# Optimization experiments

Hardware: AMD Instinct MI355X
Metric: run time of the kernel (lower is better)

Reference implementation:

```python
import jax, jax.numpy as jnp
from jax import lax
import numpy as np

B, L1, L2 = 64, 1024, 1024


def setup_inputs() -> dict:
    key = jax.random.key(0)
    ks = jax.random.split(key, 6)
    s1 = 1.0 / np.sqrt(L1)
    s2 = 1.0 / np.sqrt(L2)
    return {
        "a": jax.random.normal(ks[0], (B, L1), dtype=jnp.float32),
        "b": jax.random.normal(ks[1], (B, L2), dtype=jnp.float32),
        # nn.Linear(L1, L1) and nn.Linear(L2, L2) params (PyTorch default uniform init range)
        "W1": jax.random.uniform(ks[2], (L1, L1), jnp.float32, -s1, s1),
        "b1": jax.random.uniform(ks[3], (L1,), jnp.float32, -s1, s1),
        "W2": jax.random.uniform(ks[4], (L2, L2), jnp.float32, -s2, s2),
        "b2": jax.random.uniform(ks[5], (L2,), jnp.float32, -s2, s2),
    }


def _dtw_cost(cost):
    """DTW accumulated-cost DP for one [N, M] pairwise-cost matrix.

    R[i,j] = cost[i,j] + min(R[i-1,j-1], R[i-1,j], R[i,j-1]).
    The within-row dependency x[j] = c[j] + min(m[j], x[j-1]) is a min-plus
    prefix: x[j] = S[j] + cummin(m - S_{j-1}) with S = cumsum(c), which lets
    each row be computed in parallel (wavefront-equivalent vectorization).
    Returns the scalar DTW distance R[N-1, M-1].
    """
    dt = cost.dtype
    row0 = jnp.cumsum(cost[0])  # R[0, :]

    def step(prev_row, c_row):
        # m[j] = min(R[i-1, j], R[i-1, j-1]);  j=0 has no (i-1, j-1) neighbor
        shifted = jnp.concatenate([jnp.full((1,), jnp.inf, dt), prev_row[:-1]])
        m = jnp.minimum(prev_row, shifted)
        S = jnp.cumsum(c_row)
        S_prev = jnp.concatenate([jnp.zeros((1,), dt), S[:-1]])
        row = S + lax.associative_scan(jnp.minimum, m - S_prev)
        return row, None

    last_row, _ = lax.scan(step, row0, cost[1:])
    return last_row[-1]


def reference(a, b, W1, b1, W2, b2):
    # seq1 / seq2 linear projections over the time axis
    a_p = a @ W1.T + b1  # [B, L1]
    b_p = b @ W2.T + b2  # [B, L2]
    # squared-euclidean pairwise cost (scipy.sqeuclidean on scalar elements)
    cost = (a_p[:, :, None] - b_p[:, None, :]) ** 2  # [B, L1, L2]
    return jax.vmap(_dtw_cost)(cost)  # [B] DTW distances
```

## Files before the change

### kernel.cpp

```cpp
#include <hip/hip_runtime.h>
#include <math.h>


#define L 1024
#define BATCH 64

__global__ __launch_bounds__(256) void proj_kernel(
    const float* __restrict__ a, const float* __restrict__ b,
    const float* __restrict__ W1, const float* __restrict__ b1,
    const float* __restrict__ W2, const float* __restrict__ b2,
    float* __restrict__ ap, float* __restrict__ bp, int KC) {
  int part = blockIdx.x >> 7;
  int sub = blockIdx.x & 127;
  const float* X;
  const float* W;
  const float* bias;
  float* out;
  int i0;
  if (sub < 64) {
    X = a; W = W1; bias = b1; out = ap + part * BATCH * L; i0 = sub * 16;
  } else {
    X = b; W = W2; bias = b2; out = bp + part * BATCH * L; i0 = (sub - 64) * 16;
  }

  __shared__ float a_s[64][33];
  __shared__ float w_s[16][33];

  int tid = threadIdx.x;
  int lane_b = tid & 63;
  int iq = tid >> 6;

  float acc[4] = {0.f, 0.f, 0.f, 0.f};

  int kbeg = part * KC;
  int kend = kbeg + KC;
  for (int k0 = kbeg; k0 < kend; k0 += 32) {
    {
      int row = tid >> 2;
      int kl = (tid & 3) * 8;
      const float4* src = reinterpret_cast<const float4*>(&X[row * L + k0 + kl]);
      float4 v0 = src[0];
      float4 v1 = src[1];
      a_s[row][kl + 0] = v0.x; a_s[row][kl + 1] = v0.y;
      a_s[row][kl + 2] = v0.z; a_s[row][kl + 3] = v0.w;
      a_s[row][kl + 4] = v1.x; a_s[row][kl + 5] = v1.y;
      a_s[row][kl + 6] = v1.z; a_s[row][kl + 7] = v1.w;
    }
    {
      int row = tid >> 4;
      int kl = (tid & 15) * 2;
      float2 v = *reinterpret_cast<const float2*>(&W[(i0 + row) * L + k0 + kl]);
      w_s[row][kl] = v.x;
      w_s[row][kl + 1] = v.y;
    }
    __syncthreads();
    #pragma unroll 8
    for (int kl = 0; kl < 32; ++kl) {
      float av = a_s[lane_b][kl];
      #pragma unroll
      for (int m = 0; m < 4; ++m) {
        acc[m] += av * w_s[iq * 4 + m][kl];
      }
    }
    __syncthreads();
  }

  #pragma unroll
  for (int m = 0; m < 4; ++m) {
    int i = i0 + iq * 4 + m;
    float bv = (part == 0) ? bias[i] : 0.f;
    out[lane_b * L + i] = acc[m] + bv;
  }
}


#define NW 4
#define CPL 4
#define KBAR 32
#define OFF 95
#define DMAX (OFF * (NW - 1) + 63)
#define NG 43
#define NSTEPS (NG * KBAR)
#define APPAD (DMAX + NSTEPS + 64)

__device__ __forceinline__ float dpp_shr1(float v, float old) {
  int r = __builtin_amdgcn_update_dpp(__float_as_int(old), __float_as_int(v),
                                      0x138, 0xf, 0xf, false);
  return __int_as_float(r);
}

__device__ __forceinline__ float dpp_shl1(float v) {
  int r = __builtin_amdgcn_update_dpp(__float_as_int(v), __float_as_int(v),
                                      0x130, 0xf, 0xf, false);
  return __int_as_float(r);
}

__device__ __forceinline__ float min3f(float x, float y, float z) {
  float r;
  asm("v_min3_f32 %0, %1, %2, %3" : "=v"(r) : "v"(x), "v"(y), "v"(z));
  return r;
}

__global__ __launch_bounds__(256) void dtw_kernel(const float* __restrict__ app,
                                                  const float* __restrict__ bpp,
                                                  float* __restrict__ out,
                                                  int parts) {
  const int b = blockIdx.x;
  const int tid = threadIdx.x;
  const int w = tid >> 6;
  const int t = tid & 63;
  const int woff = w * OFF;
  const int D = woff + t;
  const float INF = INFINITY;

  __shared__ float ap_pad[APPAD];
  __shared__ float ring[NW - 1][64];

  for (int idx = tid; idx < APPAD; idx += 256) {
    int src = idx - DMAX;
    float v = 0.f;
    if ((unsigned)src < (unsigned)L) {
      v = app[b * L + src];
      for (int p = 1; p < parts; ++p) v += app[p * BATCH * L + b * L + src];
    }
    ap_pad[idx] = v;
  }

  float4 bv = *reinterpret_cast<const float4*>(&bpp[b * L + tid * CPL]);
  for (int p = 1; p < parts; ++p) {
    float4 u = *reinterpret_cast<const float4*>(
        &bpp[p * BATCH * L + b * L + tid * CPL]);
    bv.x += u.x; bv.y += u.y; bv.z += u.z; bv.w += u.w;
  }
  const float bpv0 = bv.x, bpv1 = bv.y, bpv2 = bv.z, bpv3 = bv.w;

  float p0 = INF, p1 = INF, p2 = INF, p3 = INF;
  float right = INF, prev_left = INF;
  float vprod = INF;
  float ringchunk = (w == 0 && t == 0) ? 0.f : INF;
  const float* apl = &ap_pad[DMAX - D];

  __syncthreads();

#define DTW_GROUP(s0v, PRED, FIRSTG)                                         \
  {                                                                          \
    const int s0 = (s0v);                                                    \
    float apf[KBAR];                                                         \
    _Pragma("unroll")                                                        \
    for (int k = 0; k < KBAR; ++k) apf[k] = apl[s0 + k];                     \
    if (w > 0 && t < KBAR)                                                   \
      ringchunk = ring[w - 1][(s0 - woff + t) & 63];                         \
    _Pragma("unroll")                                                        \
    for (int k = 0; k < KBAR; ++k) {                                         \
      float left = dpp_shr1(right, ringchunk);                               \
      ringchunk = dpp_shl1(ringchunk);                                       \
      int ii = s0 + k - D;                                                   \
      if (!(PRED) || ((unsigned)ii < (unsigned)L)) {                         \
        float dprev = prev_left;                                             \
        if ((FIRSTG) && k == 1 && w == 0 && t == 0) dprev = INF;             \
        prev_left = left;                                                    \
        float apv = apf[k];                                                  \
        float d0 = apv - bpv0, d1 = apv - bpv1;                              \
        float d2 = apv - bpv2, d3 = apv - bpv3;                              \
        float x = left, bb;                                                  \
        bb = min3f(p0, dprev, x); x = __builtin_fmaf(d0, d0, bb);            \
        dprev = p0; p0 = x;                                                  \
        bb = min3f(p1, dprev, x); x = __builtin_fmaf(d1, d1, bb);            \
        dprev = p1; p1 = x;                                                  \
        bb = min3f(p2, dprev, x); x = __builtin_fmaf(d2, d2, bb);            \
        dprev = p2; p2 = x;                                                  \
        bb = min3f(p3, dprev, x); x = __builtin_fmaf(d3, d3, bb);            \
        p3 = x;                                                              \
        right = x;                                                           \
      }                                                                      \
      vprod = dpp_shl1(vprod);                                               \
      vprod = (t == 63) ? right : vprod;                                     \
    }                                                                        \
    if (w < NW - 1 && t >= 64 - KBAR)                                        \
      ring[w][(s0 + t - woff - (63 + KBAR)) & 63] = vprod;                   \
    __syncthreads();                                                         \
  }

  for (int g = 0; g < 11; ++g) DTW_GROUP(g * KBAR, true, g == 0);
  for (int g = 11; g < 32; ++g) DTW_GROUP(g * KBAR, false, false);
  for (int g = 32; g < NG; ++g) DTW_GROUP(g * KBAR, true, false);
#undef DTW_GROUP

  if (tid == NW * 64 - 1) out[b] = right;
}

extern "C" void kernel_launch(void* const* d_in, const int* in_sizes, int n_in,
                              void* d_out, int out_size, void* d_ws, size_t ws_size,
                              hipStream_t stream) {
  const float* a  = (const float*)d_in[0];
  const float* b  = (const float*)d_in[1];
  const float* W1 = (const float*)d_in[2];
  const float* b1 = (const float*)d_in[3];
  const float* W2 = (const float*)d_in[4];
  const float* b2 = (const float*)d_in[5];
  float* out = (float*)d_out;

  size_t per_part = (size_t)2 * BATCH * L * sizeof(float);
  int parts = 1;
  if (ws_size >= 4 * per_part) parts = 4;
  else if (ws_size >= 2 * per_part) parts = 2;

  float* ap = (float*)d_ws;
  float* bp = ap + (size_t)parts * BATCH * L;

  proj_kernel<<<128 * parts, 256, 0, stream>>>(a, b, W1, b1, W2, b2,
                                               ap, bp, L / parts);
  dtw_kernel<<<BATCH, 256, 0, stream>>>(ap, bp, out, parts);
}
```

Before: 99.11 us.

## Process two DTW rows per wavefront step to halve anti-diagonal sweep length

Each thread now computes a 2x4 block of DTW cells per step (two consecutive rows of `a` against its four `b` columns) instead of 1x4. Wavefront steps drop from 43 to 27 groups. The ring exchange between waves becomes float2, and the padded `a` buffer is laid out as row pairs. In exchange each step has a longer dependent chain of min3/fma and higher register pressure, which `launch_bounds(256,1)` is meant to accommodate.

```diff
diff --git a/kernel.cpp b/kernel.cpp
--- a/kernel.cpp
+++ b/kernel.cpp
@@ -78,10 +78,11 @@
 #define CPL 4
 #define KBAR 32
 #define OFF 95
-#define DMAX (OFF * (NW - 1) + 63)
-#define NG 43
+#define DMAXS (OFF * (NW - 1) + 63)
+#define NG 27
 #define NSTEPS (NG * KBAR)
-#define APPAD (DMAX + NSTEPS + 64)
+#define ROWPAD (2 * DMAXS)
+#define APPAD (ROWPAD + 2 * NSTEPS + 8)
 
 __device__ __forceinline__ float dpp_shr1(float v, float old) {
   int r = __builtin_amdgcn_update_dpp(__float_as_int(old), __float_as_int(v),
@@ -101,10 +102,9 @@
   return r;
 }
 
-__global__ __launch_bounds__(256) void dtw_kernel(const float* __restrict__ app,
-                                                  const float* __restrict__ bpp,
-                                                  float* __restrict__ out,
-                                                  int parts) {
+__global__ __launch_bounds__(256, 1) void dtw_kernel(
+    const float* __restrict__ app, const float* __restrict__ bpp,
+    float* __restrict__ out, int parts) {
   const int b = blockIdx.x;
   const int tid = threadIdx.x;
   const int w = tid >> 6;
@@ -114,10 +114,10 @@
   const float INF = INFINITY;
 
   __shared__ float ap_pad[APPAD];
-  __shared__ float ring[NW - 1][64];
+  __shared__ float2 ring2[NW - 1][64];
 
   for (int idx = tid; idx < APPAD; idx += 256) {
-    int src = idx - DMAX;
+    int src = idx - ROWPAD;
     float v = 0.f;
     if ((unsigned)src < (unsigned)L) {
       v = app[b * L + src];
@@ -135,58 +135,69 @@
   const float bpv0 = bv.x, bpv1 = bv.y, bpv2 = bv.z, bpv3 = bv.w;
 
   float p0 = INF, p1 = INF, p2 = INF, p3 = INF;
-  float right = INF, prev_left = INF;
-  float vprod = INF;
-  float ringchunk = (w == 0 && t == 0) ? 0.f : INF;
-  const float* apl = &ap_pad[DMAX - D];
+  float e0 = INF, e1 = INF;
+  float prev_l1 = (w == 0 && t == 0) ? 0.f : INF;
+  float rc0 = INF, rc1 = INF;
+  float vp0 = INF, vp1 = INF;
+
+  const float2* apl2 =
+      reinterpret_cast<const float2*>(ap_pad + (ROWPAD - 2 * D));
 
   __syncthreads();
 
-#define DTW_GROUP(s0v, PRED, FIRSTG)                                         \
+#define DTW_GROUP(s0v, PRED)                                                 \
   {                                                                          \
     const int s0 = (s0v);                                                    \
-    float apf[KBAR];                                                         \
+    float2 apf[KBAR];                                                        \
     _Pragma("unroll")                                                        \
-    for (int k = 0; k < KBAR; ++k) apf[k] = apl[s0 + k];                     \
-    if (w > 0 && t < KBAR)                                                   \
-      ringchunk = ring[w - 1][(s0 - woff + t) & 63];                         \
+    for (int k = 0; k < KBAR; ++k) apf[k] = apl2[s0 + k];                    \
+    if (w > 0 && t < KBAR) {                                                 \
+      float2 rr = ring2[w - 1][(s0 - woff + t) & 63];                        \
+      rc0 = rr.x; rc1 = rr.y;                                                \
+    }                                                                        \
     _Pragma("unroll")                                                        \
     for (int k = 0; k < KBAR; ++k) {                                         \
-      float left = dpp_shr1(right, ringchunk);                               \
-      ringchunk = dpp_shl1(ringchunk);                                       \
+      float l0 = dpp_shr1(e0, rc0);                                          \
+      float l1 = dpp_shr1(e1, rc1);                                          \
+      rc0 = dpp_shl1(rc0);                                                   \
+      rc1 = dpp_shl1(rc1);                                                   \
       int ii = s0 + k - D;                                                   \
-      if (!(PRED) || ((unsigned)ii < (unsigned)L)) {                         \
-        float dprev = prev_left;                                             \
-        if ((FIRSTG) && k == 1 && w == 0 && t == 0) dprev = INF;             \
-        prev_left = left;                                                    \
-        float apv = apf[k];                                                  \
-        float d0 = apv - bpv0, d1 = apv - bpv1;                              \
-        float d2 = apv - bpv2, d3 = apv - bpv3;                              \
-        float x = left, bb;                                                  \
-        bb = min3f(p0, dprev, x); x = __builtin_fmaf(d0, d0, bb);            \
-        dprev = p0; p0 = x;                                                  \
-        bb = min3f(p1, dprev, x); x = __builtin_fmaf(d1, d1, bb);            \
-        dprev = p1; p1 = x;                                                  \
-        bb = min3f(p2, dprev, x); x = __builtin_fmaf(d2, d2, bb);            \
-        dprev = p2; p2 = x;                                                  \
-        bb = min3f(p3, dprev, x); x = __builtin_fmaf(d3, d3, bb);            \
-        p3 = x;                                                              \
-        right = x;                                                           \
+      if (!(PRED) || ((unsigned)ii < 512u)) {                                \
+        float a0 = apf[k].x, a1 = apf[k].y;                                  \
+        float d00 = a0 - bpv0, d01 = a0 - bpv1;                              \
+        float d02 = a0 - bpv2, d03 = a0 - bpv3;                              \
+        float d10 = a1 - bpv0, d11 = a1 - bpv1;                              \
+        float d12 = a1 - bpv2, d13 = a1 - bpv3;                              \
+        float x00 = __builtin_fmaf(d00, d00, min3f(p0, prev_l1, l0));        \
+        float x01 = __builtin_fmaf(d01, d01, min3f(p1, p0, x00));            \
+        float x02 = __builtin_fmaf(d02, d02, min3f(p2, p1, x01));            \
+        float x03 = __builtin_fmaf(d03, d03, min3f(p3, p2, x02));            \
+        float x10 = __builtin_fmaf(d10, d10, min3f(x00, l0, l1));            \
+        float x11 = __builtin_fmaf(d11, d11, min3f(x01, x00, x10));          \
+        float x12 = __builtin_fmaf(d12, d12, min3f(x02, x01, x11));          \
+        float x13 = __builtin_fmaf(d13, d13, min3f(x03, x02, x12));          \
+        p0 = x10; p1 = x11; p2 = x12; p3 = x13;                              \
+        prev_l1 = l1;                                                        \
+        e0 = x03; e1 = x13;                                                  \
       }                                                                      \
-      vprod = dpp_shl1(vprod);                                               \
-      vprod = (t == 63) ? right : vprod;                                     \
+      vp0 = dpp_shl1(vp0);                                                   \
+      vp0 = (t == 63) ? e0 : vp0;                                            \
+      vp1 = dpp_shl1(vp1);                                                   \
+      vp1 = (t == 63) ? e1 : vp1;                                            \
     }                                                                        \
-    if (w < NW - 1 && t >= 64 - KBAR)                                        \
-      ring[w][(s0 + t - woff - (63 + KBAR)) & 63] = vprod;                   \
+    if (w < NW - 1 && t >= 64 - KBAR) {                                      \
+      float2 st; st.x = vp0; st.y = vp1;                                     \
+      ring2[w][(s0 + t - woff - (63 + KBAR)) & 63] = st;                     \
+    }                                                                        \
     __syncthreads();                                                         \
   }
 
-  for (int g = 0; g < 11; ++g) DTW_GROUP(g * KBAR, true, g == 0);
-  for (int g = 11; g < 32; ++g) DTW_GROUP(g * KBAR, false, false);
-  for (int g = 32; g < NG; ++g) DTW_GROUP(g * KBAR, true, false);
+  for (int g = 0; g < 11; ++g) DTW_GROUP(g * KBAR, true);
+  for (int g = 11; g < 16; ++g) DTW_GROUP(g * KBAR, false);
+  for (int g = 16; g < NG; ++g) DTW_GROUP(g * KBAR, true);
 #undef DTW_GROUP
 
-  if (tid == NW * 64 - 1) out[b] = right;
+  if (tid == NW * 64 - 1) out[b] = p3;
 }
 
 extern "C" void kernel_launch(void* const* d_in, const int* in_sizes, int n_in,
```

Result: slower. 106.7 us (+7.7%).
